# Kernel tuning notes

Measured on AMD Instinct MI355X. Metric: run time of the kernel, lower is better.

The kernel has to match this reference:

```python
import jax, jax.numpy as jnp
import numpy as np

N_NODES = 1_000_000
N_EDGES = 32_000_000

def setup_inputs() -> dict:
    key = jax.random.key(0)
    ks = jax.random.split(key, 7)
    x = jax.random.normal(ks[0], (N_NODES, 1), dtype=jnp.float32)
    edge_index = jax.random.randint(ks[1], (2, N_EDGES), 0, N_NODES, dtype=jnp.int32)
    W1 = jax.random.normal(ks[2], (1, 4), dtype=jnp.float32)
    b1 = jax.random.normal(ks[3], (4,), dtype=jnp.float32)
    W2 = jax.random.normal(ks[4], (4, 1), dtype=jnp.float32)
    b2 = jax.random.normal(ks[5], (1,), dtype=jnp.float32)
    Wsage = jax.random.normal(ks[6], (1, 1), dtype=jnp.float32)
    return {"x": x, "edge_index": edge_index, "W1": W1, "b1": b1,
            "W2": W2, "b2": b2, "Wsage": Wsage}

def reference(x, edge_index, W1, b1, W2, b2, Wsage):
    # MLP: Linear(1,4) -> ReLU -> Linear(4,1)
    h = jax.nn.relu(x @ W1 + b1) @ W2 + b2  # [N,1]
    # SAGEConv(1,1, root_weight=False, bias=False): mean-aggregate neighbors, then linear
    src, dst = edge_index[0], edge_index[1]
    n = h.shape[0]
    msgs = jnp.take(h, src, axis=0)                       # [E,1] gather
    summed = jax.ops.segment_sum(msgs, dst, num_segments=n)  # [N,1]
    cnt = jax.ops.segment_sum(jnp.ones((msgs.shape[0], 1), h.dtype), dst, num_segments=n)
    mean = summed / jnp.maximum(cnt, 1.0)                 # isolated nodes -> 0
    return mean @ Wsage
```

## Files before the change

kernel.cpp:

```cpp
#include <hip/hip_runtime.h>

__global__ void node_mlp_kernel(const float* __restrict__ x,
                                const float* __restrict__ W1,
                                const float* __restrict__ b1,
                                const float* __restrict__ W2,
                                const float* __restrict__ b2,
                                float* __restrict__ h, int N) {
    const float w10 = W1[0], w11 = W1[1], w12 = W1[2], w13 = W1[3];
    const float b10 = b1[0], b11 = b1[1], b12 = b1[2], b13 = b1[3];
    const float w20 = W2[0], w21 = W2[1], w22 = W2[2], w23 = W2[3];
    const float b2v = b2[0];
    int i = blockIdx.x * blockDim.x + threadIdx.x;
    if (i < N) {
        float xv = x[i];
        float acc = b2v;
        acc += fmaxf(fmaf(xv, w10, b10), 0.0f) * w20;
        acc += fmaxf(fmaf(xv, w11, b11), 0.0f) * w21;
        acc += fmaxf(fmaf(xv, w12, b12), 0.0f) * w22;
        acc += fmaxf(fmaf(xv, w13, b13), 0.0f) * w23;
        h[i] = acc;
    }
}

#define NBINS    256
#define NSUB     8
#define BIN_CAP  131072
#define SUBCAP   (BIN_CAP / NSUB)
#define CHUNK    4096
#define BLK      256
#define EPT      16
#define MAGIC_SH 42
#define PBITS    12
#define SRCBITS  20

__global__ void init_cursor_kernel(int* __restrict__ cursor) {
    int t = blockIdx.x * blockDim.x + threadIdx.x;
    if (t < NBINS * NSUB) cursor[t] = (t >> 3) * BIN_CAP + (t & (NSUB - 1)) * SUBCAP;
}

__device__ __forceinline__ int bin_of(int d, unsigned long long magic) {
    return (int)(((unsigned long long)(unsigned)d * magic) >> MAGIC_SH);
}

__global__ __launch_bounds__(BLK, 4)
void bin_scatter_kernel(const int* __restrict__ src,
                        const int* __restrict__ dst,
                        int* __restrict__ cursor,
                        unsigned* __restrict__ binned, int E,
                        int DIV, unsigned long long magic) {
    __shared__ int  lhist[NBINS];
    __shared__ int  lbase[NBINS];
    __shared__ int  lcur[NBINS];
    __shared__ int  gbase[NBINS];
    __shared__ int2 stage[CHUNK];

    const int t = threadIdx.x;
    lhist[t] = 0;
    __syncthreads();

    const int e0 = blockIdx.x * CHUNK;
    const int e1 = min(E, e0 + CHUNK);
    const int nval = e1 - e0;
    const int k = blockIdx.x & (NSUB - 1);

    int pk[EPT];
    #pragma unroll
    for (int it = 0; it < EPT / 4; ++it) {
        int e = e0 + 4 * (t + it * BLK);
        int4 d;
        if (e + 3 < e1) {
            d = *(const int4*)(dst + e);
        } else {
            d.x = (e + 0 < e1) ? dst[e + 0] : -1;
            d.y = (e + 1 < e1) ? dst[e + 1] : -1;
            d.z = (e + 2 < e1) ? dst[e + 2] : -1;
            d.w = (e + 3 < e1) ? dst[e + 3] : -1;
        }
        #pragma unroll
        for (int j = 0; j < 4; ++j) {
            int dd = (j == 0) ? d.x : (j == 1) ? d.y : (j == 2) ? d.z : d.w;
            int p = -1;
            if (dd >= 0) {
                int b = bin_of(dd, magic);
                p = (b << PBITS) | (dd - b * DIV);
                atomicAdd(&lhist[b], 1);
            }
            pk[4 * it + j] = p;
        }
    }
    __syncthreads();

    if (t < 64) {
        const int b4 = t * 4;
        int v[4]; int s = 0;
        #pragma unroll
        for (int j = 0; j < 4; ++j) { v[j] = lhist[b4 + j]; s += v[j]; }
        int inc = s;
        #pragma unroll
        for (int dlt = 1; dlt < 64; dlt <<= 1) {
            int u = __shfl_up(inc, dlt, 64);
            if (t >= dlt) inc += u;
        }
        int excl = inc - s;
        #pragma unroll
        for (int j = 0; j < 4; ++j) {
            lbase[b4 + j] = excl; lcur[b4 + j] = excl; excl += v[j];
        }
    }
    __syncthreads();

    int r0 = atomicAdd(&cursor[t * NSUB + k], lhist[t]);

    #pragma unroll
    for (int it = 0; it < EPT / 4; ++it) {
        int e = e0 + 4 * (t + it * BLK);
        int4 s4 = make_int4(0, 0, 0, 0);
        if (e + 3 < e1) {
            s4 = *(const int4*)(src + e);
        } else {
            if (e + 0 < e1) s4.x = src[e + 0];
            if (e + 1 < e1) s4.y = src[e + 1];
            if (e + 2 < e1) s4.z = src[e + 2];
            if (e + 3 < e1) s4.w = src[e + 3];
        }
        #pragma unroll
        for (int j = 0; j < 4; ++j) {
            int p = pk[4 * it + j];
            if (p >= 0) {
                int ss = (j == 0) ? s4.x : (j == 1) ? s4.y : (j == 2) ? s4.z : s4.w;
                int slot = atomicAdd(&lcur[p >> PBITS], 1);
                stage[slot] = make_int2(p, ss);
            }
        }
    }
    gbase[t] = r0;
    __syncthreads();

    const int subend_off = (k + 1) * SUBCAP;
    for (int i = t; i < nval; i += BLK) {
        int2 ent = stage[i];
        int b = ent.x >> PBITS;
        int addr = gbase[b] + (i - lbase[b]);
        if (addr < b * BIN_CAP + subend_off)
            binned[addr] = ((unsigned)(ent.x & ((1 << PBITS) - 1)) << SRCBITS)
                           | (unsigned)ent.y;
    }
}

#define RBLK 1024

__global__ __launch_bounds__(RBLK)
void bin_reduce_kernel(const unsigned* __restrict__ binned,
                       const int* __restrict__ cursor,
                       const float* __restrict__ h,
                       const float* __restrict__ Wsage,
                       float* __restrict__ out, int N, int DIV) {
    extern __shared__ unsigned long long acc[];
    const int b = blockIdx.x;
    const int t = threadIdx.x;
    for (int i = t; i < DIV; i += RBLK) acc[i] = 0ULL;
    __syncthreads();

    const unsigned smask = (1u << SRCBITS) - 1;
    #pragma unroll 1
    for (int k = 0; k < NSUB; ++k) {
        const int sub_base = b * BIN_CAP + k * SUBCAP;
        int count = cursor[b * NSUB + k] - sub_base;
        if (count > SUBCAP) count = SUBCAP;

        const uint4* sub4 = (const uint4*)(binned + sub_base);
        const int nquad = count >> 2;
        for (int i = t; i < nquad; i += RBLK) {
            uint4 p = sub4[i];
            #pragma unroll
            for (int j = 0; j < 4; ++j) {
                unsigned e = (j == 0) ? p.x : (j == 1) ? p.y : (j == 2) ? p.z : p.w;
                float hv = h[e & smask];
                long long v = (long long)llrintf(hv * 65536.0f);
                atomicAdd(&acc[e >> SRCBITS], (unsigned long long)((1LL << 32) + v));
            }
        }
        int tail = count & 3;
        if (t < tail) {
            unsigned e = binned[sub_base + (nquad << 2) + t];
            float hv = h[e & smask];
            long long v = (long long)llrintf(hv * 65536.0f);
            atomicAdd(&acc[e >> SRCBITS], (unsigned long long)((1LL << 32) + v));
        }
    }
    __syncthreads();

    const float ws = Wsage[0];
    const int n0 = b * DIV;
    for (int i = t; i < DIV; i += RBLK) {
        int n = n0 + i;
        if (n < N) {
            long long T = (long long)acc[i];
            long long cnt = (T + (1LL << 31)) >> 32;
            long long sf  = T - (cnt << 32);
            float sum = (float)sf * (1.0f / 65536.0f);
            float c   = (float)cnt;
            out[n] = (sum / fmaxf(c, 1.0f)) * ws;
        }
    }
}

#define PACK_C 4294967296.0

__global__ void edge_scatter_kernel(const int* __restrict__ src,
                                    const int* __restrict__ dst,
                                    const float* __restrict__ h,
                                    double* __restrict__ acc, int E) {
    int tid = blockIdx.x * blockDim.x + threadIdx.x;
    int nthreads = gridDim.x * blockDim.x;
    int E4 = E >> 2;
    const int4* src4 = (const int4*)src;
    const int4* dst4 = (const int4*)dst;
    for (int i = tid; i < E4; i += nthreads) {
        int4 s = src4[i];
        int4 d = dst4[i];
        unsafeAtomicAdd(&acc[d.x], (double)h[s.x] + PACK_C);
        unsafeAtomicAdd(&acc[d.y], (double)h[s.y] + PACK_C);
        unsafeAtomicAdd(&acc[d.z], (double)h[s.z] + PACK_C);
        unsafeAtomicAdd(&acc[d.w], (double)h[s.w] + PACK_C);
    }
    for (int e = (E4 << 2) + tid; e < E; e += nthreads)
        unsafeAtomicAdd(&acc[dst[e]], (double)h[src[e]] + PACK_C);
}

__global__ void finalize_kernel(const double* __restrict__ acc,
                                const float* __restrict__ Wsage,
                                float* __restrict__ out, int N) {
    const float ws = Wsage[0];
    int i = blockIdx.x * blockDim.x + threadIdx.x;
    if (i < N) {
        double t = acc[i];
        double cd = floor(t * (1.0 / PACK_C) + 0.5);
        double sd = t - cd * PACK_C;
        out[i] = (float)(sd / (double)fmaxf((float)cd, 1.0f)) * ws;
    }
}

extern "C" void kernel_launch(void* const* d_in, const int* in_sizes, int n_in,
                              void* d_out, int out_size, void* d_ws, size_t ws_size,
                              hipStream_t stream) {
    const float* x     = (const float*)d_in[0];
    const int*   edge  = (const int*)d_in[1];
    const float* W1    = (const float*)d_in[2];
    const float* b1    = (const float*)d_in[3];
    const float* W2    = (const float*)d_in[4];
    const float* b2    = (const float*)d_in[5];
    const float* Wsage = (const float*)d_in[6];

    const int N = in_sizes[0];
    const int E = in_sizes[1] / 2;
    const int* src = edge;
    const int* dst = edge + E;

    const int DIV = (N + NBINS - 1) / NBINS;
    const unsigned long long magic =
        ((1ULL << MAGIC_SH) + (unsigned long long)DIV - 1) / (unsigned long long)DIV;

    size_t off_h      = 0;
    size_t off_cursor = off_h + (size_t)N * sizeof(float);
    size_t off_binned = (off_cursor + (size_t)NBINS * NSUB * sizeof(int) + 255) & ~(size_t)255;
    size_t need = off_binned + (size_t)NBINS * BIN_CAP * sizeof(unsigned);

    float* h = (float*)((char*)d_ws + off_h);

    node_mlp_kernel<<<(N + BLK - 1) / BLK, BLK, 0, stream>>>(x, W1, b1, W2, b2, h, N);

    if (ws_size >= need && DIV < (1 << PBITS) && N <= (1 << SRCBITS)) {
        int*      cursor = (int*)((char*)d_ws + off_cursor);
        unsigned* binned = (unsigned*)((char*)d_ws + off_binned);

        init_cursor_kernel<<<(NBINS * NSUB + BLK - 1) / BLK, BLK, 0, stream>>>(cursor);

        int nchunks = (E + CHUNK - 1) / CHUNK;
        bin_scatter_kernel<<<nchunks, BLK, 0, stream>>>(src, dst, cursor, binned, E,
                                                        DIV, magic);

        size_t lds_bytes = (size_t)DIV * sizeof(unsigned long long);
        bin_reduce_kernel<<<NBINS, RBLK, lds_bytes, stream>>>(binned, cursor, h, Wsage,
                                                              (float*)d_out, N, DIV);
    } else {
        double* acc = (double*)((char*)d_ws + ((off_cursor + 7) & ~(size_t)7));
        hipMemsetAsync(acc, 0, (size_t)N * sizeof(double), stream);
        edge_scatter_kernel<<<2048, BLK, 0, stream>>>(src, dst, h, acc, E);
        finalize_kernel<<<(N + BLK - 1) / BLK, BLK, 0, stream>>>(acc, Wsage, (float*)d_out, N);
    }
}
```

Before: 352.6 us.

## Split per-bin reduction across two blocks with partial buffers and finalize pass

Each destination bin's sub-buckets are now split between two blocks, each accumulating into its own LDS histogram and writing 64-bit packed partials to workspace. A separate finalize kernel sums the two partials, decodes count and fixed-point sum, and writes the mean times Wsage. The aim is to double the grid of the reduction stage so more blocks run per CU and gather latency is better hidden. The cost is extra global traffic for the partials and one more kernel launch, with a fallback to the old single-block reduce if the workspace is too small.

```diff
diff --git a/kernel.cpp b/kernel.cpp
--- a/kernel.cpp
+++ b/kernel.cpp
@@ -147,7 +147,80 @@
     }
 }
 
-#define RBLK 1024
+#define RBLK   1024
+#define RSPLIT 2
+#define SUBS_PER_BLK (NSUB / RSPLIT)
+
+__global__ __launch_bounds__(RBLK)
+void bin_reduce_partial_kernel(const unsigned* __restrict__ binned,
+                               const int* __restrict__ cursor,
+                               const float* __restrict__ h,
+                               unsigned long long* __restrict__ partial,
+                               int DIV) {
+    extern __shared__ unsigned long long acc[];
+    const int blk  = blockIdx.x;
+    const int b    = blk >> 1;
+    const int half = blk & 1;
+    const int t = threadIdx.x;
+    for (int i = t; i < DIV; i += RBLK) acc[i] = 0ULL;
+    __syncthreads();
+
+    const unsigned smask = (1u << SRCBITS) - 1;
+    #pragma unroll 1
+    for (int kk = 0; kk < SUBS_PER_BLK; ++kk) {
+        const int k = half * SUBS_PER_BLK + kk;
+        const int sub_base = b * BIN_CAP + k * SUBCAP;
+        int count = cursor[b * NSUB + k] - sub_base;
+        if (count > SUBCAP) count = SUBCAP;
+
+        const uint4* sub4 = (const uint4*)(binned + sub_base);
+        const int nquad = count >> 2;
+        for (int i = t; i < nquad; i += RBLK) {
+            uint4 p = sub4[i];
+            #pragma unroll
+            for (int j = 0; j < 4; ++j) {
+                unsigned e = (j == 0) ? p.x : (j == 1) ? p.y : (j == 2) ? p.z : p.w;
+                float hv = h[e & smask];
+                long long v = (long long)llrintf(hv * 65536.0f);
+                atomicAdd(&acc[e >> SRCBITS], (unsigned long long)((1LL << 32) + v));
+            }
+        }
+        int tail = count & 3;
+        if (t < tail) {
+            unsigned e = binned[sub_base + (nquad << 2) + t];
+            float hv = h[e & smask];
+            long long v = (long long)llrintf(hv * 65536.0f);
+            atomicAdd(&acc[e >> SRCBITS], (unsigned long long)((1LL << 32) + v));
+        }
+    }
+    __syncthreads();
+
+    unsigned long long* dstp = partial + (size_t)blk * DIV;
+    for (int i = t; i < DIV; i += RBLK) dstp[i] = acc[i];
+}
+
+__global__ __launch_bounds__(RBLK)
+void bin_finalize_kernel(const unsigned long long* __restrict__ partial,
+                         const float* __restrict__ Wsage,
+                         float* __restrict__ out, int N, int DIV) {
+    const float ws = Wsage[0];
+    const int b = blockIdx.x;
+    const int t = threadIdx.x;
+    const unsigned long long* p0 = partial + (size_t)(2 * b) * DIV;
+    const unsigned long long* p1 = p0 + DIV;
+    const int n0 = b * DIV;
+    for (int i = t; i < DIV; i += RBLK) {
+        int n = n0 + i;
+        if (n < N) {
+            long long T = (long long)(p0[i] + p1[i]);
+            long long cnt = (T + (1LL << 31)) >> 32;
+            long long sf  = T - (cnt << 32);
+            float sum = (float)sf * (1.0f / 65536.0f);
+            float c   = (float)cnt;
+            out[n] = (sum / fmaxf(c, 1.0f)) * ws;
+        }
+    }
+}
 
 __global__ __launch_bounds__(RBLK)
 void bin_reduce_kernel(const unsigned* __restrict__ binned,
@@ -167,7 +240,6 @@
         const int sub_base = b * BIN_CAP + k * SUBCAP;
         int count = cursor[b * NSUB + k] - sub_base;
         if (count > SUBCAP) count = SUBCAP;
-
         const uint4* sub4 = (const uint4*)(binned + sub_base);
         const int nquad = count >> 2;
         for (int i = t; i < nquad; i += RBLK) {
@@ -261,16 +333,18 @@
     const unsigned long long magic =
         ((1ULL << MAGIC_SH) + (unsigned long long)DIV - 1) / (unsigned long long)DIV;
 
-    size_t off_h      = 0;
-    size_t off_cursor = off_h + (size_t)N * sizeof(float);
-    size_t off_binned = (off_cursor + (size_t)NBINS * NSUB * sizeof(int) + 255) & ~(size_t)255;
-    size_t need = off_binned + (size_t)NBINS * BIN_CAP * sizeof(unsigned);
+    size_t off_h       = 0;
+    size_t off_cursor  = off_h + (size_t)N * sizeof(float);
+    size_t off_binned  = (off_cursor + (size_t)NBINS * NSUB * sizeof(int) + 255) & ~(size_t)255;
+    size_t off_partial = (off_binned + (size_t)NBINS * BIN_CAP * sizeof(unsigned) + 255) & ~(size_t)255;
+    size_t need_nosplit = off_partial;
+    size_t need_full    = off_partial + (size_t)NBINS * RSPLIT * DIV * sizeof(unsigned long long);
 
     float* h = (float*)((char*)d_ws + off_h);
 
     node_mlp_kernel<<<(N + BLK - 1) / BLK, BLK, 0, stream>>>(x, W1, b1, W2, b2, h, N);
 
-    if (ws_size >= need && DIV < (1 << PBITS) && N <= (1 << SRCBITS)) {
+    if (ws_size >= need_nosplit && DIV < (1 << PBITS) && N <= (1 << SRCBITS)) {
         int*      cursor = (int*)((char*)d_ws + off_cursor);
         unsigned* binned = (unsigned*)((char*)d_ws + off_binned);
 
@@ -281,8 +355,18 @@
                                                         DIV, magic);
 
         size_t lds_bytes = (size_t)DIV * sizeof(unsigned long long);
-        bin_reduce_kernel<<<NBINS, RBLK, lds_bytes, stream>>>(binned, cursor, h, Wsage,
-                                                              (float*)d_out, N, DIV);
+        if (ws_size >= need_full) {
+            unsigned long long* partial =
+                (unsigned long long*)((char*)d_ws + off_partial);
+            bin_reduce_partial_kernel<<<NBINS * RSPLIT, RBLK, lds_bytes, stream>>>(
+                binned, cursor, h, partial, DIV);
+            bin_finalize_kernel<<<NBINS, RBLK, 0, stream>>>(partial, Wsage,
+                                                            (float*)d_out, N, DIV);
+        } else {
+            bin_reduce_kernel<<<NBINS, RBLK, lds_bytes, stream>>>(binned, cursor, h,
+                                                                  Wsage, (float*)d_out,
+                                                                  N, DIV);
+        }
     } else {
         double* acc = (double*)((char*)d_ws + ((off_cursor + 7) & ~(size_t)7));
         hipMemsetAsync(acc, 0, (size_t)N * sizeof(double), stream);
```

New measurement: 359.7 us. +2.0%, slower.
